# Performance work log

Hardware: AMD Instinct MI355X
Metric: run time of the kernel (lower is better)

Reference implementation:

```python
import jax, jax.numpy as jnp
import numpy as np

CIN, COUT, KH, KW = 128, 256, 3, 3

def setup_inputs() -> dict:
    key = jax.random.key(0)
    kx, kw = jax.random.split(key)
    x = jax.random.normal(kx, (32, CIN, 56, 56), dtype=jnp.float32)
    # kaiming normal, fan_in mode, relu gain: std = sqrt(2 / fan_in)
    fan_in = CIN * KH * KW
    weight = jax.random.normal(kw, (COUT, CIN, KH, KW), dtype=jnp.float32) * jnp.sqrt(2.0 / fan_in)
    bias = jnp.zeros((COUT,), dtype=jnp.float32)
    return {"x": x, "weight": weight, "bias": bias}

def reference(x, weight, bias):
    # VALID 2D cross-correlation (matches torch conv semantics of the manual loop)
    y = jax.lax.conv_general_dilated(
        x, weight,
        window_strides=(1, 1),
        padding="VALID",
        dimension_numbers=("NCHW", "OIHW", "NCHW"),
    )
    return y + bias[None, :, None, None]
```

## Files before the change

kernel.cpp:

```cpp
#include <hip/hip_runtime.h>
#include <hip/hip_bf16.h>

#define CIN 128
#define COUT 256
#define H 56
#define W 56
#define OH 54
#define OW 54

typedef __attribute__((ext_vector_type(8))) short short8;
typedef __attribute__((ext_vector_type(4))) float floatx4;

typedef __attribute__((address_space(3))) unsigned int  lds_u32;
typedef const __attribute__((address_space(1))) unsigned int glb_u32;

static __device__ __forceinline__ unsigned short f2bf(float f) {
  unsigned int u = __builtin_bit_cast(unsigned int, f);
  u += 0x7fffu + ((u >> 16) & 1u);
  return (unsigned short)(u >> 16);
}

__global__ void repack_w(const float* __restrict__ w, unsigned short* __restrict__ w2) {
  int idx = blockIdx.x * 256 + threadIdx.x;
  if (idx >= COUT * CIN * 9) return;
  int kw = idx % 3, t1 = idx / 3;
  int kh = t1 % 3, t2 = t1 / 3;
  int ci = t2 % CIN;
  int co = t2 / CIN;
  int c8 = ci >> 3, j = ci & 7;
  w2[((((kh * 3 + kw) * 16 + c8) * COUT + co) * 8) + j] = f2bf(w[idx]);
}

__global__ __launch_bounds__(256) void repack_x(const float* __restrict__ x,
                                                unsigned short* __restrict__ xb) {
  __shared__ float xt[56][129];
  const int h = blockIdx.x;
  const int n = blockIdx.y;
  const float* src = x + (size_t)n * CIN * (H * W) + h * W;
  #pragma unroll
  for (int r = 0; r < 28; ++r) {
    int idx = r * 256 + threadIdx.x;
    int ci = idx / 56, iw = idx % 56;
    xt[iw][ci] = src[ci * (H * W) + iw];
  }
  __syncthreads();
  unsigned short* dst = xb + ((size_t)n * H + h) * 896 * 8;
  #pragma unroll
  for (int r = 0; r < 4; ++r) {
    int g = r * 256 + threadIdx.x;
    if (g < 896) {
      int iw = g >> 4, c16 = g & 15;
      short8 v;
      #pragma unroll
      for (int j = 0; j < 8; ++j)
        v[j] = (short)f2bf(xt[iw][c16 * 8 + j]);
      int gp = iw * 16 + (c16 ^ (iw & 7));
      *reinterpret_cast<short8*>(&dst[gp * 8]) = v;
    }
  }
}

__global__ __launch_bounds__(256, 2) void conv7(
    const unsigned short* __restrict__ xb, const unsigned short* __restrict__ w2,
    const float* __restrict__ bias, float* __restrict__ out) {
  __shared__ alignas(16) unsigned short xs[3744 * 8];

  const int f = blockIdx.x;
  const int swz = (f & 7) * 108 + (f >> 3);
  const int ohp = swz % 27;
  const int n   = swz / 27;
  const int oh0 = ohp * 2;
  const int tid = threadIdx.x;
  const int wid  = tid >> 6;
  const int lane = tid & 63;

  {
    const unsigned short* src = xb + ((size_t)n * H + oh0) * 896 * 8;
    #pragma unroll
    for (int i = 0; i < 14; ++i) {
      int idx = (wid * 14 + i) * 64;
      __builtin_amdgcn_global_load_lds(
          (glb_u32*)(src + (size_t)(idx + lane) * 8),
          (lds_u32*)(&xs[idx * 8]), 16, 0, 0);
    }
  }
  asm volatile("s_waitcnt vmcnt(0)" ::: "memory");
  __syncthreads();

  const int wm   = wid >> 1;
  const int wn   = wid & 1;
  const int l16  = lane & 15;
  const int cig  = lane >> 4;
  const int co_base = wm * 128;
  const int oh = oh0 + wn;
  const int rowd = cig * 4;

  floatx4 acc[8][4];
  #pragma unroll
  for (int m = 0; m < 8; ++m)
    #pragma unroll
    for (int nr = 0; nr < 4; ++nr)
      acc[m][nr] = (floatx4){0.f, 0.f, 0.f, 0.f};

  #pragma unroll
  for (int s = 0; s < 36; ++s) {
    const int kh = s / 12, ch = (s / 3) & 3, kw = s % 3;
    const int row = wn + kh;
    const unsigned short* wp =
        w2 + ((size_t)(((kh * 3 + kw) * 16 + (ch * 4 + cig)) * COUT + co_base + l16)) * 8;
    short8 a[8];
    #pragma unroll
    for (int m = 0; m < 8; ++m)
      a[m] = *reinterpret_cast<const short8*>(wp + m * 128);
    const int iwl = l16 + kw;
    const int c16x = (ch * 4 + cig) ^ (iwl & 7);
    const int boff = (row * 896 + iwl * 16 + c16x) * 8;
    short8 b[4];
    #pragma unroll
    for (int nr = 0; nr < 4; ++nr)
      b[nr] = *reinterpret_cast<const short8*>(&xs[boff + nr * 2048]);

    __builtin_amdgcn_s_setprio(1);
    #pragma unroll
    for (int m = 0; m < 8; ++m)
      #pragma unroll
      for (int nr = 0; nr < 4; ++nr)
        acc[m][nr] = __builtin_amdgcn_mfma_f32_16x16x32_bf16(a[m], b[nr], acc[m][nr], 0, 0, 0);
    __builtin_amdgcn_s_setprio(0);
  }

  #pragma unroll
  for (int m = 0; m < 8; ++m) {
    #pragma unroll
    for (int reg = 0; reg < 4; ++reg) {
      int co = co_base + m * 16 + rowd + reg;
      float bvv = bias[co];
      float* op = out + (((size_t)n * COUT + co) * OH + oh) * OW;
      #pragma unroll
      for (int nr = 0; nr < 4; ++nr) {
        int ow = nr * 16 + l16;
        if (ow < OW) op[ow] = acc[m][nr][reg] + bvv;
      }
    }
  }
}

#define CSTR 136
#define IWP 66

__global__ __launch_bounds__(512, 4) void conv_fb(
    const float* __restrict__ x, const unsigned short* __restrict__ w2,
    const float* __restrict__ bias, float* __restrict__ out) {
  __shared__ alignas(16) unsigned short xsf[4 * IWP * CSTR];

  const int ohp = blockIdx.x;
  const int n   = blockIdx.y;
  const int oh0 = ohp * 2;
  const int tid = threadIdx.x;

  {
    short8 zz = {0, 0, 0, 0, 0, 0, 0, 0};
    for (int i = tid; i < 4 * 10 * 17; i += 512) {
      int r = i / 170, rem = i % 170;
      int iw = 56 + rem / 17, g = rem % 17;
      *reinterpret_cast<short8*>(&xsf[(r * IWP + iw) * CSTR + g * 8]) = zz;
    }
  }
  for (int s = tid; s < 3584; s += 512) {
    int iw = s % 56;
    int t  = s / 56;
    int c8 = t & 15, r = t >> 4;
    const float* xp = x + (size_t)n * CIN * (H * W) + (oh0 + r) * W + iw;
    short8 v;
    #pragma unroll
    for (int j = 0; j < 8; ++j)
      v[j] = (short)f2bf(xp[(size_t)(c8 * 8 + j) * (H * W)]);
    *reinterpret_cast<short8*>(&xsf[(r * IWP + iw) * CSTR + c8 * 8]) = v;
  }
  __syncthreads();

  const int wid  = tid >> 6;
  const int lane = tid & 63;
  const int wm   = wid >> 1;
  const int wn   = wid & 1;
  const int l16  = lane & 15;
  const int cig  = lane >> 4;

  const int co_base = wm * 64;
  const int oh = oh0 + wn;

  floatx4 acc[4][4];
  #pragma unroll
  for (int m = 0; m < 4; ++m)
    #pragma unroll
    for (int nr = 0; nr < 4; ++nr)
      acc[m][nr] = (floatx4){0.f, 0.f, 0.f, 0.f};

  for (int kh = 0; kh < 3; ++kh) {
    const int row = wn + kh;
    #pragma unroll
    for (int ch = 0; ch < 4; ++ch) {
      const int bbase = (row * IWP + l16) * CSTR + ch * 32 + cig * 8;
      #pragma unroll
      for (int kw = 0; kw < 3; ++kw) {
        const unsigned short* wp =
            w2 + ((size_t)(((kh * 3 + kw) * 16 + (ch * 4 + cig)) * COUT + co_base + l16)) * 8;
        short8 a[4];
        #pragma unroll
        for (int m = 0; m < 4; ++m)
          a[m] = *reinterpret_cast<const short8*>(wp + m * 16 * 8);
        short8 b[4];
        #pragma unroll
        for (int nr = 0; nr < 4; ++nr)
          b[nr] = *reinterpret_cast<const short8*>(&xsf[bbase + (nr * 16 + kw) * CSTR]);
        #pragma unroll
        for (int m = 0; m < 4; ++m)
          #pragma unroll
          for (int nr = 0; nr < 4; ++nr)
            acc[m][nr] = __builtin_amdgcn_mfma_f32_16x16x32_bf16(a[m], b[nr], acc[m][nr], 0, 0, 0);
      }
    }
  }

  const int rowd = cig * 4;
  #pragma unroll
  for (int m = 0; m < 4; ++m) {
    #pragma unroll
    for (int reg = 0; reg < 4; ++reg) {
      int co = co_base + m * 16 + rowd + reg;
      float bvv = bias[co];
      float* op = out + (((size_t)n * COUT + co) * OH + oh) * OW;
      #pragma unroll
      for (int nr = 0; nr < 4; ++nr) {
        int ow = nr * 16 + l16;
        if (ow < OW) op[ow] = acc[m][nr][reg] + bvv;
      }
    }
  }
}

extern "C" void kernel_launch(void* const* d_in, const int* in_sizes, int n_in,
                              void* d_out, int out_size, void* d_ws, size_t ws_size,
                              hipStream_t stream) {
  (void)in_sizes; (void)n_in; (void)out_size;
  const float* x    = (const float*)d_in[0];
  const float* w    = (const float*)d_in[1];
  const float* bias = (const float*)d_in[2];
  float* out = (float*)d_out;

  const size_t W2_BYTES = (size_t)9 * 16 * COUT * 8 * 2;
  const size_t XB_BYTES = (size_t)32 * H * 896 * 8 * 2;
  unsigned short* w2 = (unsigned short*)d_ws;

  repack_w<<<dim3((COUT * CIN * 9 + 255) / 256), dim3(256), 0, stream>>>(w, w2);

  if (ws_size >= W2_BYTES + XB_BYTES) {
    unsigned short* xb = (unsigned short*)((char*)d_ws + W2_BYTES);
    repack_x<<<dim3(56, 32), dim3(256), 0, stream>>>(x, xb);
    conv7<<<dim3(864), dim3(256), 0, stream>>>(xb, w2, bias, out);
  } else {
    conv_fb<<<dim3(27, 32), dim3(512), 0, stream>>>(x, w2, bias, out);
  }
}
```

Baseline: 95.52 us.

## Flatten two output rows into 7 pixel fragments to cut padded MFMA waste

Each wave now covers 64 output channels and the full 108 pixels of the block's two output rows, packed as seven 16-wide fragments. Before, each wave handled 128 channels and one row padded to 64 columns. MFMA count per wave drops from 32 to 28 per step, removing work spent on padded columns. In exchange, the per-fragment LDS addresses are computed from row/column tables, and each wave loads more B fragments but fewer A fragments per step. Some output stores become less regular across the row boundary.

New measurement: 84.97 us. -11.0%, faster.

```diff
diff --git a/kernel.cpp b/kernel.cpp
--- a/kernel.cpp
+++ b/kernel.cpp
@@ -60,7 +60,7 @@
   }
 }
 
-__global__ __launch_bounds__(256, 2) void conv7(
+__global__ __launch_bounds__(256, 2) void conv8(
     const unsigned short* __restrict__ xb, const unsigned short* __restrict__ w2,
     const float* __restrict__ bias, float* __restrict__ out) {
   __shared__ alignas(16) unsigned short xs[3744 * 8];
@@ -87,59 +87,66 @@
   asm volatile("s_waitcnt vmcnt(0)" ::: "memory");
   __syncthreads();
 
-  const int wm   = wid >> 1;
-  const int wn   = wid & 1;
   const int l16  = lane & 15;
   const int cig  = lane >> 4;
-  const int co_base = wm * 128;
-  const int oh = oh0 + wn;
+  const int co_base = wid * 64;
   const int rowd = cig * 4;
 
-  floatx4 acc[8][4];
-  #pragma unroll
-  for (int m = 0; m < 8; ++m)
-    #pragma unroll
-    for (int nr = 0; nr < 4; ++nr)
-      acc[m][nr] = (floatx4){0.f, 0.f, 0.f, 0.f};
+  int rp[7], owp[7];
+  #pragma unroll
+  for (int fr = 0; fr < 7; ++fr) {
+    int p = fr * 16 + l16;
+    rp[fr]  = (p < 54) ? 0 : 1;
+    owp[fr] = p - rp[fr] * 54;
+  }
+
+  floatx4 acc[4][7];
+  #pragma unroll
+  for (int m = 0; m < 4; ++m)
+    #pragma unroll
+    for (int fr = 0; fr < 7; ++fr)
+      acc[m][fr] = (floatx4){0.f, 0.f, 0.f, 0.f};
 
   #pragma unroll
   for (int s = 0; s < 36; ++s) {
     const int kh = s / 12, ch = (s / 3) & 3, kw = s % 3;
-    const int row = wn + kh;
     const unsigned short* wp =
         w2 + ((size_t)(((kh * 3 + kw) * 16 + (ch * 4 + cig)) * COUT + co_base + l16)) * 8;
-    short8 a[8];
-    #pragma unroll
-    for (int m = 0; m < 8; ++m)
+    short8 a[4];
+    #pragma unroll
+    for (int m = 0; m < 4; ++m)
       a[m] = *reinterpret_cast<const short8*>(wp + m * 128);
-    const int iwl = l16 + kw;
-    const int c16x = (ch * 4 + cig) ^ (iwl & 7);
-    const int boff = (row * 896 + iwl * 16 + c16x) * 8;
-    short8 b[4];
-    #pragma unroll
-    for (int nr = 0; nr < 4; ++nr)
-      b[nr] = *reinterpret_cast<const short8*>(&xs[boff + nr * 2048]);
+    const int chb = ch * 4 + cig;
+    short8 b[7];
+    #pragma unroll
+    for (int fr = 0; fr < 7; ++fr) {
+      const int iwl = owp[fr] + kw;
+      const int c16x = chb ^ (iwl & 7);
+      const int boff = ((rp[fr] + kh) * 896 + iwl * 16 + c16x) * 8;
+      b[fr] = *reinterpret_cast<const short8*>(&xs[boff]);
+    }
 
     __builtin_amdgcn_s_setprio(1);
     #pragma unroll
-    for (int m = 0; m < 8; ++m)
-      #pragma unroll
-      for (int nr = 0; nr < 4; ++nr)
-        acc[m][nr] = __builtin_amdgcn_mfma_f32_16x16x32_bf16(a[m], b[nr], acc[m][nr], 0, 0, 0);
+    for (int m = 0; m < 4; ++m)
+      #pragma unroll
+      for (int fr = 0; fr < 7; ++fr)
+        acc[m][fr] = __builtin_amdgcn_mfma_f32_16x16x32_bf16(a[m], b[fr], acc[m][fr], 0, 0, 0);
     __builtin_amdgcn_s_setprio(0);
   }
 
   #pragma unroll
-  for (int m = 0; m < 8; ++m) {
+  for (int m = 0; m < 4; ++m) {
     #pragma unroll
     for (int reg = 0; reg < 4; ++reg) {
       int co = co_base + m * 16 + rowd + reg;
       float bvv = bias[co];
-      float* op = out + (((size_t)n * COUT + co) * OH + oh) * OW;
-      #pragma unroll
-      for (int nr = 0; nr < 4; ++nr) {
-        int ow = nr * 16 + l16;
-        if (ow < OW) op[ow] = acc[m][nr][reg] + bvv;
+      float* opb = out + (((size_t)n * COUT + co) * OH + oh0) * OW;
+      #pragma unroll
+      for (int fr = 0; fr < 7; ++fr) {
+        int p = fr * 16 + l16;
+        if (p < 108)
+          opb[rp[fr] * OW + owp[fr]] = acc[m][fr][reg] + bvv;
       }
     }
   }
@@ -257,7 +264,7 @@
   if (ws_size >= W2_BYTES + XB_BYTES) {
     unsigned short* xb = (unsigned short*)((char*)d_ws + W2_BYTES);
     repack_x<<<dim3(56, 32), dim3(256), 0, stream>>>(x, xb);
-    conv7<<<dim3(864), dim3(256), 0, stream>>>(xb, w2, bias, out);
+    conv8<<<dim3(864), dim3(256), 0, stream>>>(xb, w2, bias, out);
   } else {
     conv_fb<<<dim3(27, 32), dim3(512), 0, stream>>>(x, w2, bias, out);
   }
```
